# Kernel optimization log

Measured on AMD Instinct MI355X. Metric: run time of the kernel, lower is better.

The kernel has to match this reference:

```python
import jax, jax.numpy as jnp
import numpy as np

IN_FEATURES = 4096
OUT_FEATURES = 11008
TOKENS = 32


def ternarize_weight(w):
    # abs-mean scale, clamped; threshold at 0.7*abs_mean
    abs_mean = jnp.maximum(jnp.mean(jnp.abs(w)), 1e-5)
    threshold = 0.7 * abs_mean
    q = jnp.where(w > threshold, 1.0, jnp.where(w < -threshold, -1.0, 0.0))
    # straight-through estimator: forward value q*abs_mean, grad passes to w
    return w + jax.lax.stop_gradient(q * abs_mean - w)


def setup_inputs() -> dict:
    key = jax.random.key(0)
    kx, kw = jax.random.split(key)
    x = jax.random.normal(kx, (TOKENS, IN_FEATURES), dtype=jnp.float32)
    # master fp32 weights, init std = 1/sqrt(in_features) as in the module
    weight = jax.random.normal(kw, (OUT_FEATURES, IN_FEATURES), dtype=jnp.float32) / np.sqrt(IN_FEATURES)
    return {"x": x, "weight": weight}


def reference(x, weight):
    # ternary_active=True, ternary_alpha=1.0 path: fully ternarized weights
    w_q = ternarize_weight(weight)
    # F.linear(x, w): [T, in] @ [out, in]^T -> [T, out]
    return jnp.einsum('ti,oi->to', x, w_q)
```

## Files before the change

kernel.cpp:

```cpp
#include <hip/hip_runtime.h>
#include <hip/hip_bf16.h>
#include <stdint.h>

#define IN_F 4096
#define OUT_F 11008
#define TOKENS 32
#define NELEM_W (OUT_F * IN_F)
#define OUT_ELEMS (TOKENS * OUT_F)
#define NBLK 688

typedef __attribute__((ext_vector_type(8))) __bf16 bf16x8;
typedef __attribute__((ext_vector_type(4))) float  f32x4;

#define APART_OFF 0
#define XB_OFF    4096

__device__ __forceinline__ uint32_t bfr(float v) {
    uint32_t u = __float_as_uint(v);
    uint32_t r = u + 0x7FFFu + ((u >> 16) & 1u);
    return r >> 16;
}

__global__ __launch_bounds__(256) void absum_xcvt_kernel(const float* __restrict__ w,
                                                         const float* __restrict__ x,
                                                         float* __restrict__ apart,
                                                         uint4* __restrict__ xb) {
    const int tid = threadIdx.x;
    if (blockIdx.x < 64) {
        int i = blockIdx.x * 256 + tid;
        const float4* x4 = (const float4*)x;
        float4 a0 = x4[i * 2];
        float4 a1 = x4[i * 2 + 1];
        uint4 o;
        o.x = bfr(a0.x) | (bfr(a0.y) << 16);
        o.y = bfr(a0.z) | (bfr(a0.w) << 16);
        o.z = bfr(a1.x) | (bfr(a1.y) << 16);
        o.w = bfr(a1.z) | (bfr(a1.w) << 16);
        xb[i] = o;
    }
    const float4* wb4 = (const float4*)(w + (size_t)blockIdx.x * (16 * IN_F));
    float s = 0.f;
#pragma unroll 4
    for (int i = tid; i < 16384; i += 256) {
        float4 v = wb4[i];
        s += fabsf(v.x) + fabsf(v.y) + fabsf(v.z) + fabsf(v.w);
    }
    for (int off = 32; off > 0; off >>= 1)
        s += __shfl_down(s, off, 64);
    __shared__ float wsum[4];
    int lane = tid & 63;
    int wv   = tid >> 6;
    if (lane == 0) wsum[wv] = s;
    __syncthreads();
    if (tid == 0)
        apart[blockIdx.x] = wsum[0] + wsum[1] + wsum[2] + wsum[3];
}

__device__ __forceinline__ uint32_t tern1(float v, float thr) {
    uint32_t u  = __float_as_uint(v);
    uint32_t pm = (u & 0x80000000u) | 0x3F800000u;
    return (__builtin_fabsf(v) > thr) ? pm : 0u;
}

__device__ __forceinline__ uint2 tern4(float4 b, float thr) {
    uint32_t q0 = tern1(b.x, thr), q1 = tern1(b.y, thr);
    uint32_t q2 = tern1(b.z, thr), q3 = tern1(b.w, thr);
    uint2 r;
    r.x = __builtin_amdgcn_perm(q1, q0, 0x07060302u);
    r.y = __builtin_amdgcn_perm(q3, q2, 0x07060302u);
    return r;
}

#define CHUNKS 16
#define WAVE_LDS 2304
#define SMEM_BYTES 9216

__global__ __launch_bounds__(256, 4) void ternary_gemm(const float* __restrict__ w,
                                                       const float* __restrict__ apart,
                                                       const __bf16* __restrict__ xb,
                                                       float* __restrict__ out) {
    __shared__ char smem_raw[SMEM_BYTES];
    const int og   = blockIdx.x;
    const int tid  = threadIdx.x;
    const int wv   = tid >> 6;
    const int lane = tid & 63;
    const int col  = lane & 15;
    const int quad = lane >> 4;
    const int rlan = lane & 15;

    float s = 0.f;
    for (int j = tid; j < NBLK; j += 256) s += apart[j];
    for (int off = 32; off > 0; off >>= 1)
        s += __shfl_down(s, off, 64);
    float* sred = (float*)smem_raw;
    if (lane == 0) sred[wv] = s;
    __syncthreads();
    if (tid == 0) {
        double mean = (double)(sred[0] + sred[1] + sred[2] + sred[3]) / (double)NELEM_W;
        if (mean < 1e-5) mean = 1e-5;
        float mf = (float)mean;
        sred[4] = 0.7f * mf;
        sred[5] = mf;
    }
    __syncthreads();
    const float thr   = sred[4];
    const float scale = sred[5];
    __syncthreads();

    const int kw = wv * 1024;
    const float* wp = w + (size_t)(og * 16 + quad) * IN_F + kw + rlan * 4;
    char* stage = smem_raw + wv * WAVE_LDS;
    char* wr    = stage + quad * 144 + rlan * 8;
    const char* rd = stage + col * 144;
    const __bf16* xq = xb + (size_t)col * IN_F + kw + quad * 8;

    f32x4 acc0 = {0.f, 0.f, 0.f, 0.f};
    f32x4 acc1 = {0.f, 0.f, 0.f, 0.f};

    float4 wb[2][4];
    bf16x8 xv[2][4];

#pragma unroll
    for (int c = 0; c < 2; ++c) {
        const float*  np = wp + c * 64;
        const __bf16* xn = xq + c * 64;
        wb[c][0] = *(const float4*)(np);
        wb[c][1] = *(const float4*)(np + 4 * IN_F);
        wb[c][2] = *(const float4*)(np + 8 * IN_F);
        wb[c][3] = *(const float4*)(np + 12 * IN_F);
        xv[c][0] = *(const bf16x8*)(xn);
        xv[c][1] = *(const bf16x8*)(xn + 32);
        xv[c][2] = *(const bf16x8*)(xn + 16 * IN_F);
        xv[c][3] = *(const bf16x8*)(xn + 16 * IN_F + 32);
    }

#define GEMM_BODY(c, cur)                                                      \
    {                                                                          \
        uint2 t0 = tern4(wb[cur][0], thr);                                     \
        uint2 t1 = tern4(wb[cur][1], thr);                                     \
        uint2 t2 = tern4(wb[cur][2], thr);                                     \
        uint2 t3 = tern4(wb[cur][3], thr);                                     \
        *(uint2*)(wr)        = t0;                                             \
        *(uint2*)(wr + 576)  = t1;                                             \
        *(uint2*)(wr + 1152) = t2;                                             \
        *(uint2*)(wr + 1728) = t3;                                             \
        bf16x8 a00 = xv[cur][0], a01 = xv[cur][1];                             \
        bf16x8 a10 = xv[cur][2], a11 = xv[cur][3];                             \
        if ((c) + 2 < CHUNKS) {                                                \
            const float*  np = wp + ((c) + 2) * 64;                            \
            const __bf16* xn = xq + ((c) + 2) * 64;                            \
            wb[cur][0] = *(const float4*)(np);                                 \
            wb[cur][1] = *(const float4*)(np + 4 * IN_F);                      \
            wb[cur][2] = *(const float4*)(np + 8 * IN_F);                      \
            wb[cur][3] = *(const float4*)(np + 12 * IN_F);                     \
            xv[cur][0] = *(const bf16x8*)(xn);                                 \
            xv[cur][1] = *(const bf16x8*)(xn + 32);                            \
            xv[cur][2] = *(const bf16x8*)(xn + 16 * IN_F);                     \
            xv[cur][3] = *(const bf16x8*)(xn + 16 * IN_F + 32);                \
        }                                                                      \
        bf16x8 bw0 = *(const bf16x8*)(rd + quad * 16);                         \
        bf16x8 bw1 = *(const bf16x8*)(rd + 64 + quad * 16);                    \
        acc0 = __builtin_amdgcn_mfma_f32_16x16x32_bf16(a00, bw0, acc0, 0, 0, 0); \
        acc1 = __builtin_amdgcn_mfma_f32_16x16x32_bf16(a10, bw0, acc1, 0, 0, 0); \
        acc0 = __builtin_amdgcn_mfma_f32_16x16x32_bf16(a01, bw1, acc0, 0, 0, 0); \
        acc1 = __builtin_amdgcn_mfma_f32_16x16x32_bf16(a11, bw1, acc1, 0, 0, 0); \
    }

    for (int c = 0; c < CHUNKS; c += 2) {
        GEMM_BODY(c, 0)
        GEMM_BODY(c + 1, 1)
    }
#undef GEMM_BODY

    __syncthreads();
    float* red  = (float*)smem_raw;
    float* base = red + wv * 512;
#pragma unroll
    for (int r = 0; r < 4; ++r) base[r * 64 + lane]       = acc0[r];
#pragma unroll
    for (int r = 0; r < 4; ++r) base[256 + r * 64 + lane] = acc1[r];
    __syncthreads();

#pragma unroll
    for (int p = tid; p < 512; p += 256) {
        int t = p >> 4, cc = p & 15;
        int a = t >> 4;
        int q = (t >> 2) & 3;
        int r = t & 3;
        int idx = a * 256 + r * 64 + q * 16 + cc;
        float v = red[idx] + red[512 + idx] + red[1024 + idx] + red[1536 + idx];
        out[(size_t)t * OUT_F + og * 16 + cc] = v * scale;
    }
}

extern "C" void kernel_launch(void* const* d_in, const int* in_sizes, int n_in,
                              void* d_out, int out_size, void* d_ws, size_t ws_size,
                              hipStream_t stream) {
    const float* x = (const float*)d_in[0];
    const float* w = (const float*)d_in[1];
    float* out     = (float*)d_out;
    char* ws       = (char*)d_ws;

    float* apart   = (float*)(ws + APART_OFF);
    uint4* xb      = (uint4*)(ws + XB_OFF);

    absum_xcvt_kernel<<<NBLK, 256, 0, stream>>>(w, x, apart, xb);
    ternary_gemm<<<NBLK, 256, 0, stream>>>(w, apart, (const __bf16*)(ws + XB_OFF), out);
}
```

Measured before the change: 282.6 us.

## Fuse abs-sum and ternary GEMM into one cooperative persistent kernel

Merges the weight abs-sum/x-conversion kernel and the ternary GEMM into a single cooperative kernel launched with 256 blocks, with a grid-wide sync between the reduction and the GEMM phases. Each block then loops over about 2.7 output groups persistently. This is meant to remove a kernel launch and its boundary gap. In exchange it adds a grid barrier, gives the GEMM phase less parallelism (256 blocks on 256 CUs, uneven 3/2 groups per block), and makes the reduction use grid-stride access instead of contiguous slabs.

```diff
diff --git a/kernel.cpp b/kernel.cpp
--- a/kernel.cpp
+++ b/kernel.cpp
@@ -1,13 +1,16 @@
 #include <hip/hip_runtime.h>
 #include <hip/hip_bf16.h>
+#include <hip/hip_cooperative_groups.h>
 #include <stdint.h>
+
+namespace cg = cooperative_groups;
 
 #define IN_F 4096
 #define OUT_F 11008
 #define TOKENS 32
 #define NELEM_W (OUT_F * IN_F)
-#define OUT_ELEMS (TOKENS * OUT_F)
-#define NBLK 688
+#define NBLK 256
+#define NOG 688
 
 typedef __attribute__((ext_vector_type(8))) __bf16 bf16x8;
 typedef __attribute__((ext_vector_type(4))) float  f32x4;
@@ -21,13 +24,38 @@
     return r >> 16;
 }
 
-__global__ __launch_bounds__(256) void absum_xcvt_kernel(const float* __restrict__ w,
-                                                         const float* __restrict__ x,
-                                                         float* __restrict__ apart,
-                                                         uint4* __restrict__ xb) {
-    const int tid = threadIdx.x;
-    if (blockIdx.x < 64) {
-        int i = blockIdx.x * 256 + tid;
+__device__ __forceinline__ uint32_t tern1(float v, float thr) {
+    uint32_t u  = __float_as_uint(v);
+    uint32_t pm = (u & 0x80000000u) | 0x3F800000u;
+    return (__builtin_fabsf(v) > thr) ? pm : 0u;
+}
+
+__device__ __forceinline__ uint2 tern4(float4 b, float thr) {
+    uint32_t q0 = tern1(b.x, thr), q1 = tern1(b.y, thr);
+    uint32_t q2 = tern1(b.z, thr), q3 = tern1(b.w, thr);
+    uint2 r;
+    r.x = __builtin_amdgcn_perm(q1, q0, 0x07060302u);
+    r.y = __builtin_amdgcn_perm(q3, q2, 0x07060302u);
+    return r;
+}
+
+#define CHUNKS 16
+#define WAVE_LDS 2304
+#define SMEM_BYTES 9216
+
+__global__ __launch_bounds__(256) void fused_kernel(const float* __restrict__ w,
+                                                    const float* __restrict__ x,
+                                                    float* __restrict__ apart,
+                                                    uint4* __restrict__ xb,
+                                                    float* __restrict__ out) {
+    __shared__ char smem_raw[SMEM_BYTES];
+    const int bid  = blockIdx.x;
+    const int tid  = threadIdx.x;
+    const int wv   = tid >> 6;
+    const int lane = tid & 63;
+
+    if (bid < 64) {
+        int i = bid * 256 + tid;
         const float4* x4 = (const float4*)x;
         float4 a0 = x4[i * 2];
         float4 a1 = x4[i * 2 + 1];
@@ -38,62 +66,34 @@
         o.w = bfr(a1.z) | (bfr(a1.w) << 16);
         xb[i] = o;
     }
-    const float4* wb4 = (const float4*)(w + (size_t)blockIdx.x * (16 * IN_F));
-    float s = 0.f;
+
+    {
+        const float4* w4 = (const float4*)w;
+        float s = 0.f;
 #pragma unroll 4
-    for (int i = tid; i < 16384; i += 256) {
-        float4 v = wb4[i];
-        s += fabsf(v.x) + fabsf(v.y) + fabsf(v.z) + fabsf(v.w);
-    }
+        for (int i = bid * 256 + tid; i < NELEM_W / 4; i += NBLK * 256) {
+            float4 v = w4[i];
+            s += fabsf(v.x) + fabsf(v.y) + fabsf(v.z) + fabsf(v.w);
+        }
+        for (int off = 32; off > 0; off >>= 1)
+            s += __shfl_down(s, off, 64);
+        float* wsum = (float*)smem_raw;
+        if (lane == 0) wsum[wv] = s;
+        __syncthreads();
+        if (tid == 0)
+            apart[bid] = wsum[0] + wsum[1] + wsum[2] + wsum[3];
+    }
+
+    __threadfence();
+    cg::this_grid().sync();
+    __threadfence();
+
+    float s1 = apart[tid];
     for (int off = 32; off > 0; off >>= 1)
-        s += __shfl_down(s, off, 64);
-    __shared__ float wsum[4];
-    int lane = tid & 63;
-    int wv   = tid >> 6;
-    if (lane == 0) wsum[wv] = s;
-    __syncthreads();
-    if (tid == 0)
-        apart[blockIdx.x] = wsum[0] + wsum[1] + wsum[2] + wsum[3];
-}
-
-__device__ __forceinline__ uint32_t tern1(float v, float thr) {
-    uint32_t u  = __float_as_uint(v);
-    uint32_t pm = (u & 0x80000000u) | 0x3F800000u;
-    return (__builtin_fabsf(v) > thr) ? pm : 0u;
-}
-
-__device__ __forceinline__ uint2 tern4(float4 b, float thr) {
-    uint32_t q0 = tern1(b.x, thr), q1 = tern1(b.y, thr);
-    uint32_t q2 = tern1(b.z, thr), q3 = tern1(b.w, thr);
-    uint2 r;
-    r.x = __builtin_amdgcn_perm(q1, q0, 0x07060302u);
-    r.y = __builtin_amdgcn_perm(q3, q2, 0x07060302u);
-    return r;
-}
-
-#define CHUNKS 16
-#define WAVE_LDS 2304
-#define SMEM_BYTES 9216
-
-__global__ __launch_bounds__(256, 4) void ternary_gemm(const float* __restrict__ w,
-                                                       const float* __restrict__ apart,
-                                                       const __bf16* __restrict__ xb,
-                                                       float* __restrict__ out) {
-    __shared__ char smem_raw[SMEM_BYTES];
-    const int og   = blockIdx.x;
-    const int tid  = threadIdx.x;
-    const int wv   = tid >> 6;
-    const int lane = tid & 63;
-    const int col  = lane & 15;
-    const int quad = lane >> 4;
-    const int rlan = lane & 15;
-
-    float s = 0.f;
-    for (int j = tid; j < NBLK; j += 256) s += apart[j];
-    for (int off = 32; off > 0; off >>= 1)
-        s += __shfl_down(s, off, 64);
+        s1 += __shfl_down(s1, off, 64);
     float* sred = (float*)smem_raw;
-    if (lane == 0) sred[wv] = s;
+    __syncthreads();
+    if (lane == 0) sred[wv] = s1;
     __syncthreads();
     if (tid == 0) {
         double mean = (double)(sred[0] + sred[1] + sred[2] + sred[3]) / (double)NELEM_W;
@@ -107,39 +107,46 @@
     const float scale = sred[5];
     __syncthreads();
 
+    const int col  = lane & 15;
+    const int quad = lane >> 4;
+    const int rlan = lane & 15;
+
     const int kw = wv * 1024;
-    const float* wp = w + (size_t)(og * 16 + quad) * IN_F + kw + rlan * 4;
     char* stage = smem_raw + wv * WAVE_LDS;
     char* wr    = stage + quad * 144 + rlan * 8;
     const char* rd = stage + col * 144;
-    const __bf16* xq = xb + (size_t)col * IN_F + kw + quad * 8;
-
-    f32x4 acc0 = {0.f, 0.f, 0.f, 0.f};
-    f32x4 acc1 = {0.f, 0.f, 0.f, 0.f};
-
-    float4 wb[2][4];
-    bf16x8 xv[2][4];
-
-#pragma unroll
-    for (int c = 0; c < 2; ++c) {
-        const float*  np = wp + c * 64;
-        const __bf16* xn = xq + c * 64;
-        wb[c][0] = *(const float4*)(np);
-        wb[c][1] = *(const float4*)(np + 4 * IN_F);
-        wb[c][2] = *(const float4*)(np + 8 * IN_F);
-        wb[c][3] = *(const float4*)(np + 12 * IN_F);
-        xv[c][0] = *(const bf16x8*)(xn);
-        xv[c][1] = *(const bf16x8*)(xn + 32);
-        xv[c][2] = *(const bf16x8*)(xn + 16 * IN_F);
-        xv[c][3] = *(const bf16x8*)(xn + 16 * IN_F + 32);
-    }
+    const __bf16* xbb = (const __bf16*)xb;
+    const __bf16* xq  = xbb + (size_t)col * IN_F + kw + quad * 8;
+
+    for (int og = bid; og < NOG; og += NBLK) {
+        const float* wp = w + (size_t)(og * 16 + quad) * IN_F + kw + rlan * 4;
+
+        f32x4 acc0 = {0.f, 0.f, 0.f, 0.f};
+        f32x4 acc1 = {0.f, 0.f, 0.f, 0.f};
+
+        float4 wbuf[2][4];
+        bf16x8 xv[2][4];
+
+#pragma unroll
+        for (int c = 0; c < 2; ++c) {
+            const float*  np = wp + c * 64;
+            const __bf16* xn = xq + c * 64;
+            wbuf[c][0] = *(const float4*)(np);
+            wbuf[c][1] = *(const float4*)(np + 4 * IN_F);
+            wbuf[c][2] = *(const float4*)(np + 8 * IN_F);
+            wbuf[c][3] = *(const float4*)(np + 12 * IN_F);
+            xv[c][0] = *(const bf16x8*)(xn);
+            xv[c][1] = *(const bf16x8*)(xn + 32);
+            xv[c][2] = *(const bf16x8*)(xn + 16 * IN_F);
+            xv[c][3] = *(const bf16x8*)(xn + 16 * IN_F + 32);
+        }
 
 #define GEMM_BODY(c, cur)                                                      \
     {                                                                          \
-        uint2 t0 = tern4(wb[cur][0], thr);                                     \
-        uint2 t1 = tern4(wb[cur][1], thr);                                     \
-        uint2 t2 = tern4(wb[cur][2], thr);                                     \
-        uint2 t3 = tern4(wb[cur][3], thr);                                     \
+        uint2 t0 = tern4(wbuf[cur][0], thr);                                   \
+        uint2 t1 = tern4(wbuf[cur][1], thr);                                   \
+        uint2 t2 = tern4(wbuf[cur][2], thr);                                   \
+        uint2 t3 = tern4(wbuf[cur][3], thr);                                   \
         *(uint2*)(wr)        = t0;                                             \
         *(uint2*)(wr + 576)  = t1;                                             \
         *(uint2*)(wr + 1152) = t2;                                             \
@@ -149,10 +156,10 @@
         if ((c) + 2 < CHUNKS) {                                                \
             const float*  np = wp + ((c) + 2) * 64;                            \
             const __bf16* xn = xq + ((c) + 2) * 64;                            \
-            wb[cur][0] = *(const float4*)(np);                                 \
-            wb[cur][1] = *(const float4*)(np + 4 * IN_F);                      \
-            wb[cur][2] = *(const float4*)(np + 8 * IN_F);                      \
-            wb[cur][3] = *(const float4*)(np + 12 * IN_F);                     \
+            wbuf[cur][0] = *(const float4*)(np);                               \
+            wbuf[cur][1] = *(const float4*)(np + 4 * IN_F);                    \
+            wbuf[cur][2] = *(const float4*)(np + 8 * IN_F);                    \
+            wbuf[cur][3] = *(const float4*)(np + 12 * IN_F);                   \
             xv[cur][0] = *(const bf16x8*)(xn);                                 \
             xv[cur][1] = *(const bf16x8*)(xn + 32);                            \
             xv[cur][2] = *(const bf16x8*)(xn + 16 * IN_F);                     \
@@ -166,30 +173,32 @@
         acc1 = __builtin_amdgcn_mfma_f32_16x16x32_bf16(a11, bw1, acc1, 0, 0, 0); \
     }
 
-    for (int c = 0; c < CHUNKS; c += 2) {
-        GEMM_BODY(c, 0)
-        GEMM_BODY(c + 1, 1)
-    }
+        for (int c = 0; c < CHUNKS; c += 2) {
+            GEMM_BODY(c, 0)
+            GEMM_BODY(c + 1, 1)
+        }
 #undef GEMM_BODY
 
-    __syncthreads();
-    float* red  = (float*)smem_raw;
-    float* base = red + wv * 512;
-#pragma unroll
-    for (int r = 0; r < 4; ++r) base[r * 64 + lane]       = acc0[r];
-#pragma unroll
-    for (int r = 0; r < 4; ++r) base[256 + r * 64 + lane] = acc1[r];
-    __syncthreads();
-
-#pragma unroll
-    for (int p = tid; p < 512; p += 256) {
-        int t = p >> 4, cc = p & 15;
-        int a = t >> 4;
-        int q = (t >> 2) & 3;
-        int r = t & 3;
-        int idx = a * 256 + r * 64 + q * 16 + cc;
-        float v = red[idx] + red[512 + idx] + red[1024 + idx] + red[1536 + idx];
-        out[(size_t)t * OUT_F + og * 16 + cc] = v * scale;
+        __syncthreads();
+        float* red  = (float*)smem_raw;
+        float* base = red + wv * 512;
+#pragma unroll
+        for (int r = 0; r < 4; ++r) base[r * 64 + lane]       = acc0[r];
+#pragma unroll
+        for (int r = 0; r < 4; ++r) base[256 + r * 64 + lane] = acc1[r];
+        __syncthreads();
+
+#pragma unroll
+        for (int p = tid; p < 512; p += 256) {
+            int t = p >> 4, cc = p & 15;
+            int a = t >> 4;
+            int q = (t >> 2) & 3;
+            int r = t & 3;
+            int idx = a * 256 + r * 64 + q * 16 + cc;
+            float v = red[idx] + red[512 + idx] + red[1024 + idx] + red[1536 + idx];
+            out[(size_t)t * OUT_F + og * 16 + cc] = v * scale;
+        }
+        __syncthreads();
     }
 }
 
@@ -201,9 +210,10 @@
     float* out     = (float*)d_out;
     char* ws       = (char*)d_ws;
 
-    float* apart   = (float*)(ws + APART_OFF);
-    uint4* xb      = (uint4*)(ws + XB_OFF);
-
-    absum_xcvt_kernel<<<NBLK, 256, 0, stream>>>(w, x, apart, xb);
-    ternary_gemm<<<NBLK, 256, 0, stream>>>(w, apart, (const __bf16*)(ws + XB_OFF), out);
-}
+    float* apart = (float*)(ws + APART_OFF);
+    uint4* xb    = (uint4*)(ws + XB_OFF);
+
+    void* args[] = { (void*)&w, (void*)&x, (void*)&apart, (void*)&xb, (void*)&out };
+    hipLaunchCooperativeKernel((void*)fused_kernel, dim3(NBLK), dim3(256),
+                               args, 0, stream);
+}
```

Result: slower. 353.4 us (+25.1%).
